# Kernel tuning notes

Measured on AMD Instinct MI355X. Metric: run time of the kernel, lower is better.

Reference implementation:

```python
import jax, jax.numpy as jnp
import numpy as np

T, D = 4096, 2048
H, DK, DV = 6, 256, 512        # heads, head_k_dim, head_v_dim (expand_v=2)
KD, VD = H * DK, H * DV        # 1536, 3072
KSZ = 4                        # conv_size
GEN = D // 8                   # generator reduction 8 -> 256
EPS = 1e-5                     # norm_eps


def setup_inputs() -> dict:
    key = jax.random.key(0)
    ks = jax.random.split(key, 12)
    std = 0.02
    p = lambda i, shape: jax.random.normal(ks[i], shape, jnp.float32) * std
    rng = np.random.default_rng(0)
    A = rng.uniform(0.0, 16.0, H).astype(np.float32)
    dt = np.exp(rng.uniform(0, 1, H) * (np.log(0.1) - np.log(0.001)) + np.log(0.001)).astype(np.float32)
    dt = np.clip(dt, 1e-4, None)
    inv_dt = (dt + np.log(-np.expm1(-dt))).astype(np.float32)
    return {
        'hidden_states': jax.random.normal(ks[0], (T, D), jnp.float32),
        'Wq': p(1, (D, KD)), 'Wk': p(2, (D, KD)), 'Wv': p(3, (D, VD)),
        'Wb': p(4, (D, H)), 'Wa': p(5, (D, H)), 'Wg': p(6, (D, VD)), 'Wo': p(7, (VD, D)),
        'A_log': jnp.asarray(np.log(A)), 'dt_bias': jnp.asarray(inv_dt),
        'conv_w': p(8, (VD, KSZ)), 'gen_w1': p(9, (D, GEN)), 'gen_w2': p(10, (GEN, KSZ)),
        'norm_w': jnp.ones((DV,), jnp.float32),
    }


def _l2norm(x):
    return x * jax.lax.rsqrt(jnp.sum(x * x, -1, keepdims=True) + 1e-6)


def reference(hidden_states, Wq, Wk, Wv, Wb, Wa, Wg, Wo, A_log, dt_bias, conv_w, gen_w1, gen_w2, norm_w):
    h = hidden_states[None]                             # [1,T,D]
    q = jax.nn.silu(h @ Wq)                             # [1,T,KD]
    k = jax.nn.silu(h @ Wk)
    x = h @ Wv                                          # [1,T,VD]
    # dynamic short convolution: per-token kernel added to static depthwise kernel
    dyn = jax.nn.silu(h @ gen_w1) @ gen_w2              # [1,T,KSZ]
    xpad = jnp.pad(x, ((0, 0), (KSZ - 1, 0), (0, 0)))   # causal padding
    v = jnp.zeros_like(x)
    for j in range(KSZ):
        v = v + (conv_w[None, None, :, j] + dyn[:, :, None, j]) * xpad[:, j:j + x.shape[1], :]
    v = jax.nn.silu(v)

    B = 1
    q = _l2norm(q.reshape(B, -1, H, DK))                # use_qk_l2norm_in_kernel=True
    k = _l2norm(k.reshape(B, -1, H, DK))
    v = v.reshape(B, -1, H, DV)
    beta = jax.nn.sigmoid(h @ Wb)                       # [1,T,H]
    g = -jnp.exp(A_log) * jax.nn.softplus(h @ Wa + dt_bias)  # [1,T,H] decay log-gates
    scale = DK ** -0.5

    def step(S, inp):                                   # gated delta rule recurrence
        qt, kt, vt, gt, bt = inp
        S = S * jnp.exp(gt)[..., None, None]            # [B,H,DK,DV]
        dv = (vt - jnp.einsum('bhk,bhkv->bhv', kt, S)) * bt[..., None]
        S = S + kt[..., :, None] * dv[..., None, :]
        ot = jnp.einsum('bhk,bhkv->bhv', qt, S) * scale
        return S, ot

    S0 = jnp.zeros((B, H, DK, DV), jnp.float32)
    tm = lambda a: jnp.moveaxis(a, 1, 0)                # time-major for scan
    _, o = jax.lax.scan(step, S0, (tm(q), tm(k), tm(v), tm(g), tm(beta)))
    o = jnp.moveaxis(o, 0, 1)                           # [1,T,H,DV]

    gate = (h @ Wg).reshape(B, -1, H, DV)
    rms = jax.lax.rsqrt(jnp.mean(o * o, -1, keepdims=True) + EPS)
    o = o * rms * norm_w * jax.nn.silu(gate)            # gated RMSNorm
    o = o.reshape(B, -1, VD) @ Wo                       # [1,T,D]
    return o[0]
```

## Files before the change

### kernel.cpp

```cpp
#include <hip/hip_runtime.h>
#include <hip/hip_bf16.h>
#include <math.h>

#define T_LEN 4096
#define DIM   2048
#define NH    6
#define DK    256
#define DVh   512
#define KD    1536
#define VD    3072
#define CK    64
#define NCHK  (T_LEN / CK)

typedef __attribute__((ext_vector_type(8))) short bf16x8;
typedef __attribute__((ext_vector_type(4))) float f32x4;

__device__ __forceinline__ float silu_f(float v){ return v / (1.f + __expf(-v)); }

__device__ __forceinline__ unsigned short f2bf(float f) {
  unsigned int u = __float_as_uint(f);
  unsigned int r = u + 0x7FFFu + ((u >> 16) & 1u);
  return (unsigned short)(r >> 16);
}
__device__ __forceinline__ float bf2f(unsigned short s) {
  return __uint_as_float(((unsigned int)s) << 16);
}

__device__ __forceinline__ void bar_lds() {
  __builtin_amdgcn_sched_barrier(0);
  asm volatile("s_waitcnt lgkmcnt(0)" ::: "memory");
  __builtin_amdgcn_s_barrier();
  __builtin_amdgcn_sched_barrier(0);
}

__global__ __launch_bounds__(256) void cast_bf16(
    const float* __restrict__ in, unsigned short* __restrict__ out)
{
  int i = blockIdx.x * 256 + threadIdx.x;
  float4 v4 = ((const float4*)in)[i];
  ushort4 o4;
  o4.x = f2bf(v4.x); o4.y = f2bf(v4.y); o4.z = f2bf(v4.z); o4.w = f2bf(v4.w);
  ((ushort4*)out)[i] = o4;
}

__global__ __launch_bounds__(256) void tcast(
    const float* __restrict__ in, unsigned short* __restrict__ out, int R, int Cn)
{
  __shared__ float tile[32][33];
  int bx = blockIdx.x * 32;
  int by = blockIdx.y * 32;
  int tx = threadIdx.x & 31, ty = threadIdx.x >> 5;
#pragma unroll
  for (int i = 0; i < 32; i += 8)
    tile[ty + i][tx] = in[(size_t)(by + ty + i) * Cn + bx + tx];
  __syncthreads();
#pragma unroll
  for (int i = 0; i < 32; i += 8)
    out[(size_t)(bx + ty + i) * R + by + tx] = f2bf(tile[tx][ty + i]);
}

__global__ __launch_bounds__(256) void gemm_bt_bf16(
    const unsigned short* __restrict__ A, const unsigned short* __restrict__ BT,
    void* __restrict__ Cout, int M, int N, int K, int act)
{
  __shared__ unsigned short As[128 * 32];
  __shared__ unsigned short Bs[128 * 32];
  const int tid = threadIdx.x;
  const int bm = blockIdx.y * 128, bn = blockIdx.x * 128;
  const int lane = tid & 63, wave = tid >> 6;
  const int wm = (wave >> 1) * 64, wn = (wave & 1) * 64;
  const int fr = lane & 15, kq = lane >> 4;

  f32x4 acc[4][4];
#pragma unroll
  for (int i = 0; i < 4; ++i)
#pragma unroll
    for (int j = 0; j < 4; ++j) acc[i][j] = (f32x4){0.f, 0.f, 0.f, 0.f};

  const int r0 = tid >> 2, c0 = (tid & 3) * 8;
  const int r1 = r0 + 64;

  for (int k0 = 0; k0 < K; k0 += 32) {
    __builtin_amdgcn_global_load_lds(
        (const __attribute__((address_space(1))) unsigned int*)(A + (size_t)(bm + r0) * K + k0 + c0),
        (__attribute__((address_space(3))) unsigned int*)(As + r0 * 32 + c0), 16, 0, 0);
    __builtin_amdgcn_global_load_lds(
        (const __attribute__((address_space(1))) unsigned int*)(A + (size_t)(bm + r1) * K + k0 + c0),
        (__attribute__((address_space(3))) unsigned int*)(As + r1 * 32 + c0), 16, 0, 0);
    __builtin_amdgcn_global_load_lds(
        (const __attribute__((address_space(1))) unsigned int*)(BT + (size_t)(bn + r0) * K + k0 + c0),
        (__attribute__((address_space(3))) unsigned int*)(Bs + r0 * 32 + c0), 16, 0, 0);
    __builtin_amdgcn_global_load_lds(
        (const __attribute__((address_space(1))) unsigned int*)(BT + (size_t)(bn + r1) * K + k0 + c0),
        (__attribute__((address_space(3))) unsigned int*)(Bs + r1 * 32 + c0), 16, 0, 0);
    __syncthreads();

    bf16x8 af[4], bfr[4];
#pragma unroll
    for (int i = 0; i < 4; ++i)
      af[i] = *(const bf16x8*)(As + (wm + i * 16 + fr) * 32 + kq * 8);
#pragma unroll
    for (int j = 0; j < 4; ++j)
      bfr[j] = *(const bf16x8*)(Bs + (wn + j * 16 + fr) * 32 + kq * 8);
#pragma unroll
    for (int i = 0; i < 4; ++i)
#pragma unroll
      for (int j = 0; j < 4; ++j)
        acc[i][j] = __builtin_amdgcn_mfma_f32_16x16x32_bf16(af[i], bfr[j], acc[i][j], 0, 0, 0);
    __syncthreads();
  }

  if (act == 2) {
    unsigned short* C = (unsigned short*)Cout;
#pragma unroll
    for (int i = 0; i < 4; ++i) {
      int rbase = bm + wm + i * 16 + kq * 4;
#pragma unroll
      for (int r = 0; r < 4; ++r) {
        size_t rowoff = (size_t)(rbase + r) * N + bn + wn + fr;
#pragma unroll
        for (int j = 0; j < 4; ++j) C[rowoff + j * 16] = f2bf(acc[i][j][r]);
      }
    }
  } else {
    float* C = (float*)Cout;
#pragma unroll
    for (int i = 0; i < 4; ++i) {
      int rbase = bm + wm + i * 16 + kq * 4;
#pragma unroll
      for (int r = 0; r < 4; ++r) {
        size_t rowoff = (size_t)(rbase + r) * N + bn + wn + fr;
#pragma unroll
        for (int j = 0; j < 4; ++j) {
          float v = acc[i][j][r];
          if (act == 1) v = silu_f(v);
          C[rowoff + j * 16] = v;
        }
      }
    }
  }
}

__global__ __launch_bounds__(256) void proj_dyn(
    const float* __restrict__ tg, const float* __restrict__ w2, float* __restrict__ dyn)
{
  int t = blockIdx.x, tid = threadIdx.x;
  float g = tg[(size_t)t * 256 + tid];
  float p[4];
#pragma unroll
  for (int j = 0; j < 4; ++j) p[j] = g * w2[tid * 4 + j];
#pragma unroll
  for (int j = 0; j < 4; ++j)
    for (int m = 32; m >= 1; m >>= 1) p[j] += __shfl_xor(p[j], m);
  __shared__ float red[4][4];
  if ((tid & 63) == 0) {
    int w = tid >> 6;
#pragma unroll
    for (int j = 0; j < 4; ++j) red[w][j] = p[j];
  }
  __syncthreads();
  if (tid < 4) dyn[(size_t)t * 4 + tid] = red[0][tid] + red[1][tid] + red[2][tid] + red[3][tid];
}

__global__ __launch_bounds__(256) void proj_bg(
    const float* __restrict__ h, const float* __restrict__ Wb, const float* __restrict__ Wa,
    const float* __restrict__ A_log, const float* __restrict__ dt_bias,
    float* __restrict__ beta, float* __restrict__ gout)
{
  int t = blockIdx.x, tid = threadIdx.x;
  float pb[6], pa[6];
#pragma unroll
  for (int j = 0; j < 6; ++j) { pb[j] = 0.f; pa[j] = 0.f; }
  for (int d = tid; d < DIM; d += 256) {
    float hv = h[(size_t)t * DIM + d];
#pragma unroll
    for (int j = 0; j < 6; ++j) {
      pb[j] += hv * Wb[d * 6 + j];
      pa[j] += hv * Wa[d * 6 + j];
    }
  }
#pragma unroll
  for (int j = 0; j < 6; ++j)
    for (int m = 32; m >= 1; m >>= 1) { pb[j] += __shfl_xor(pb[j], m); pa[j] += __shfl_xor(pa[j], m); }
  __shared__ float rb[4][6], ra[4][6];
  if ((tid & 63) == 0) {
    int w = tid >> 6;
#pragma unroll
    for (int j = 0; j < 6; ++j) { rb[w][j] = pb[j]; ra[w][j] = pa[j]; }
  }
  __syncthreads();
  if (tid < 6) {
    int j = tid;
    float sb = rb[0][j] + rb[1][j] + rb[2][j] + rb[3][j];
    float sa = ra[0][j] + ra[1][j] + ra[2][j] + ra[3][j];
    beta[(size_t)t * 6 + j] = 1.f / (1.f + expf(-sb));
    float z = sa + dt_bias[j];
    float sp = (z > 20.f) ? z : log1pf(expf(z));
    gout[(size_t)t * 6 + j] = -expf(A_log[j]) * sp;
  }
}

__global__ __launch_bounds__(256) void conv_kernel(
    const float* __restrict__ x, const float* __restrict__ dyn,
    const float* __restrict__ cw, float* __restrict__ v)
{
  int c = blockIdx.x * 256 + threadIdx.x;
  int t = blockIdx.y;
  float4 w4 = ((const float4*)cw)[c];
  float d0 = dyn[t * 4 + 0], d1 = dyn[t * 4 + 1], d2 = dyn[t * 4 + 2], d3 = dyn[t * 4 + 3];
  float acc = (w4.w + d3) * x[(size_t)t * VD + c];
  if (t >= 1) acc += (w4.z + d2) * x[(size_t)(t - 1) * VD + c];
  if (t >= 2) acc += (w4.y + d1) * x[(size_t)(t - 2) * VD + c];
  if (t >= 3) acc += (w4.x + d0) * x[(size_t)(t - 3) * VD + c];
  v[(size_t)t * VD + c] = silu_f(acc);
}

__global__ __launch_bounds__(64) void l2norm_qk(
    float* __restrict__ q, float* __restrict__ k)
{
  size_t base = (size_t)blockIdx.x * 256;
  int tid = threadIdx.x;
  float4 qv = ((float4*)(q + base))[tid];
  float4 kv = ((float4*)(k + base))[tid];
  float sq = qv.x*qv.x + qv.y*qv.y + qv.z*qv.z + qv.w*qv.w;
  float sk = kv.x*kv.x + kv.y*kv.y + kv.z*kv.z + kv.w*kv.w;
  for (int m = 32; m >= 1; m >>= 1) { sq += __shfl_xor(sq, m); sk += __shfl_xor(sk, m); }
  float rq = rsqrtf(sq + 1e-6f) * 0.0625f;
  float rk = rsqrtf(sk + 1e-6f);
  qv.x *= rq; qv.y *= rq; qv.z *= rq; qv.w *= rq;
  kv.x *= rk; kv.y *= rk; kv.z *= rk; kv.w *= rk;
  ((float4*)(q + base))[tid] = qv;
  ((float4*)(k + base))[tid] = kv;
}

__global__ __launch_bounds__(64) void cumsum_g(
    const float* __restrict__ g, float* __restrict__ c, float* __restrict__ gammas)
{
  int ch = blockIdx.x, h = blockIdx.y;
  int t0 = ch * CK;
  int lane = threadIdx.x;
  float cum = g[(size_t)(t0 + lane) * 6 + h];
  for (int off = 1; off < 64; off <<= 1) {
    float n = __shfl_up(cum, off);
    if (lane >= off) cum += n;
  }
  c[(size_t)h * T_LEN + t0 + lane] = cum;
  if (lane == 63) gammas[h * NCHK + ch] = __expf(cum);
}

__global__ __launch_bounds__(384) void scale_kq(
    const float* __restrict__ q, const float* __restrict__ k, const float* __restrict__ c,
    unsigned short* __restrict__ Qb, unsigned short* __restrict__ Kb)
{
  int t = blockIdx.x;
  int tid = threadIdx.x;
  int h = tid >> 6;
  float w1 = __expf(c[(size_t)h * T_LEN + t]);
  size_t off = (size_t)t * KD + tid * 4;
  float4 qv = *(const float4*)(q + off);
  float4 kv = *(const float4*)(k + off);
  ushort4 qo, ko;
  qo.x = f2bf(w1 * qv.x); qo.y = f2bf(w1 * qv.y); qo.z = f2bf(w1 * qv.z); qo.w = f2bf(w1 * qv.w);
  ko.x = f2bf(w1 * kv.x); ko.y = f2bf(w1 * kv.y); ko.z = f2bf(w1 * kv.z); ko.w = f2bf(w1 * kv.w);
  *(ushort4*)(Qb + off) = qo;
  *(ushort4*)(Kb + off) = ko;
}

__global__ __launch_bounds__(256) void make_khT(
    const float* __restrict__ k, const float* __restrict__ c,
    unsigned short* __restrict__ KhT)
{
  int ch = blockIdx.x, h = blockIdx.y;
  int t0 = ch * CK;
  int tt = threadIdx.x & 63, ks = threadIdx.x >> 6;
  float cend = c[(size_t)h * T_LEN + t0 + 63];
  float w2 = __expf(cend - c[(size_t)h * T_LEN + t0 + tt]);
  size_t obase = ((size_t)(h * NCHK + ch)) * DK * CK;
#pragma unroll 8
  for (int kb2 = 0; kb2 < 64; ++kb2) {
    int kk = ks * 64 + kb2;
    float kv = k[(size_t)(t0 + tt) * KD + h * 256 + kk];
    KhT[obase + (size_t)kk * CK + tt] = f2bf(w2 * kv);
  }
}

__global__ __launch_bounds__(256) void chunk_lp(
    const float* __restrict__ q, const float* __restrict__ k,
    const float* __restrict__ c, const float* __restrict__ beta,
    float* __restrict__ Lg, unsigned short* __restrict__ Pm)
{
  const int ch = blockIdx.x, h = blockIdx.y;
  const int t0 = ch * CK;
  const int tid = threadIdx.x;
  const int w = tid >> 6, lane = tid & 63, fr = lane & 15, kq = lane >> 4;
  __shared__ unsigned short kb[64][264];
  __shared__ unsigned short qb[64][264];
  __shared__ float cs[64], bs[64];
#pragma unroll
  for (int i = 0; i < 16; ++i) {
    int fi = tid + i * 256;
    int r = fi >> 6, d4 = fi & 63;
    float4 kv = *(const float4*)(k + (size_t)(t0 + r) * KD + h * 256 + d4 * 4);
    float4 qv = *(const float4*)(q + (size_t)(t0 + r) * KD + h * 256 + d4 * 4);
    ushort4 k4, q4;
    k4.x = f2bf(kv.x); k4.y = f2bf(kv.y); k4.z = f2bf(kv.z); k4.w = f2bf(kv.w);
    q4.x = f2bf(qv.x); q4.y = f2bf(qv.y); q4.z = f2bf(qv.z); q4.w = f2bf(qv.w);
    *(ushort4*)&kb[r][d4 * 4] = k4;
    *(ushort4*)&qb[r][d4 * 4] = q4;
  }
  if (tid < 64) {
    cs[tid] = c[(size_t)h * T_LEN + t0 + tid];
    bs[tid] = beta[(size_t)(t0 + tid) * 6 + h];
  }
  __syncthreads();

  f32x4 akk[4], aqk[4];
#pragma unroll
  for (int j = 0; j < 4; ++j) { akk[j] = (f32x4){0,0,0,0}; aqk[j] = (f32x4){0,0,0,0}; }
#pragma unroll
  for (int kt = 0; kt < 8; ++kt) {
    bf16x8 ak = *(const bf16x8*)&kb[16 * w + fr][kt * 32 + kq * 8];
    bf16x8 aq = *(const bf16x8*)&qb[16 * w + fr][kt * 32 + kq * 8];
#pragma unroll
    for (int j = 0; j < 4; ++j) {
      bf16x8 b = *(const bf16x8*)&kb[j * 16 + fr][kt * 32 + kq * 8];
      akk[j] = __builtin_amdgcn_mfma_f32_16x16x32_bf16(ak, b, akk[j], 0, 0, 0);
      aqk[j] = __builtin_amdgcn_mfma_f32_16x16x32_bf16(aq, b, aqk[j], 0, 0, 0);
    }
  }
  size_t base = ((size_t)(h * NCHK + ch)) * CK * CK;
#pragma unroll
  for (int j = 0; j < 4; ++j) {
#pragma unroll
    for (int r = 0; r < 4; ++r) {
      int t = 16 * w + kq * 4 + r, col = j * 16 + fr;
      float e = __expf(fminf(cs[t] - cs[col], 0.f));
      Lg[base + t * 64 + col] = (col < t) ? bs[t] * e * akk[j][r] : 0.f;
      Pm[base + t * 64 + col] = f2bf((col <= t) ? e * aqk[j][r] : 0.f);
    }
  }
}

__global__ __launch_bounds__(64) void tri_inv(
    const float* __restrict__ Lg, const float* __restrict__ beta,
    unsigned short* __restrict__ Tm)
{
  const int ch = blockIdx.x, h = blockIdx.y;
  const size_t base = ((size_t)(h * NCHK + ch)) * CK * CK;
  const int j = threadIdx.x;
  __shared__ float Ll[64][65];
  __shared__ float Tl[64][65];
  for (int t = 0; t < 64; ++t) Ll[t][j] = Lg[base + t * 64 + j];
  __syncthreads();
  for (int t = 0; t < 64; ++t) {
    float s;
    if (j > t) s = 0.f;
    else if (j == t) s = 1.f;
    else {
      s = 0.f;
      for (int m = j; m < t; ++m) s -= Ll[t][m] * Tl[m][j];
    }
    Tl[t][j] = s;
  }
  float bj = beta[(size_t)(ch * 64 + j) * 6 + h];
  for (int t = 0; t < 64; ++t) Tm[base + t * 64 + j] = f2bf(Tl[t][j] * bj);
}

__global__ __launch_bounds__(256) void scan_chunk(
    const unsigned short* __restrict__ Kb,
    const unsigned short* __restrict__ Qb,
    const unsigned short* __restrict__ KhT,
    const unsigned short* __restrict__ Tm,
    const unsigned short* __restrict__ Pm,
    const float* __restrict__ gammas,
    float* __restrict__ VO)
{
  const int h = blockIdx.y, sl = blockIdx.x;
  const int tid = threadIdx.x;
  const int w = tid >> 6, lane = tid & 63;
  const int fr = lane & 15, kq = lane >> 4;

  __shared__ unsigned short S0h[16][264];
  __shared__ unsigned short S0l[16][264];
  __shared__ unsigned short XT[16][72];
  __shared__ unsigned short DVT[16][72];

  f32x4 st[4];
#pragma unroll
  for (int i = 0; i < 4; ++i) st[i] = (f32x4){0.f, 0.f, 0.f, 0.f};

  const int colg = h * DVh + sl * 16 + fr;
  const size_t hc0 = (size_t)h * NCHK;

  {
    int zr = tid >> 4;
    int zc = (tid & 15) * 16;
    ushort4 z; z.x = 0; z.y = 0; z.z = 0; z.w = 0;
#pragma unroll
    for (int u = 0; u < 4; ++u) {
      *(ushort4*)&S0h[zr][zc + 4 * u] = z;
      *(ushort4*)&S0l[zr][zc + 4 * u] = z;
    }
  }

  bf16x8 kfA[8], kfB[8], qfA[8], qfB[8];
  float vlA[4], vlB[4];

#define PREF_KQV(KF, QF, VL, chn) do { \
    const unsigned short* krow_ = Kb + (size_t)((chn) * CK + 16 * w + fr) * KD + h * 256 + kq * 8; \
    const unsigned short* qrow_ = Qb + (size_t)((chn) * CK + 16 * w + fr) * KD + h * 256 + kq * 8; \
    _Pragma("unroll") \
    for (int kt = 0; kt < 8; ++kt) { \
      KF[kt] = *(const bf16x8*)(krow_ + kt * 32); \
      QF[kt] = *(const bf16x8*)(qrow_ + kt * 32); } \
    _Pragma("unroll") \
    for (int r = 0; r < 4; ++r) VL[r] = VO[(size_t)((chn) * CK + 16 * w + kq * 4 + r) * VD + colg]; \
  } while (0)

#define CHUNK_BODY(chx, KF, QF, VL, KFN, QFN, VLN) do { \
    const int ch_ = (chx); \
    const int t0_ = ch_ * CK; \
    const size_t cb_ = hc0 + ch_; \
    bf16x8 tf[2], pf[2]; \
    { const unsigned short* trow_ = Tm + (cb_ * CK + 16 * w + fr) * CK + kq * 8; \
      const unsigned short* prow_ = Pm + (cb_ * CK + 16 * w + fr) * CK + kq * 8; \
      tf[0] = *(const bf16x8*)(trow_); tf[1] = *(const bf16x8*)(trow_ + 32); \
      pf[0] = *(const bf16x8*)(prow_); pf[1] = *(const bf16x8*)(prow_ + 32); } \
    bf16x8 hfr[4][2]; \
    _Pragma("unroll") \
    for (int i = 0; i < 4; ++i) { \
      const unsigned short* hrow_ = KhT + (cb_ * DK + 64 * w + 16 * i + fr) * CK + kq * 8; \
      hfr[i][0] = *(const bf16x8*)(hrow_); hfr[i][1] = *(const bf16x8*)(hrow_ + 32); } \
    const float gam_ = gammas[cb_]; \
     \
    { const int chn_ = (ch_ + 1 < NCHK) ? ch_ + 1 : ch_; PREF_KQV(KFN, QFN, VLN, chn_); } \
     \
     \
    f32x4 oh = (f32x4){0.f,0.f,0.f,0.f}, ol = (f32x4){0.f,0.f,0.f,0.f}; \
    { f32x4 yh = (f32x4){0.f,0.f,0.f,0.f}, yl = (f32x4){0.f,0.f,0.f,0.f}; \
      _Pragma("unroll") \
      for (int kt = 0; kt < 8; ++kt) { \
        bf16x8 bh_ = *(const bf16x8*)&S0h[fr][kt * 32 + kq * 8]; \
        bf16x8 bl_ = *(const bf16x8*)&S0l[fr][kt * 32 + kq * 8]; \
        yh = __builtin_amdgcn_mfma_f32_16x16x32_bf16(KF[kt], bh_, yh, 0, 0, 0); \
        yl = __builtin_amdgcn_mfma_f32_16x16x32_bf16(KF[kt], bl_, yl, 0, 0, 0); \
        oh = __builtin_amdgcn_mfma_f32_16x16x32_bf16(QF[kt], bh_, oh, 0, 0, 0); \
        ol = __builtin_amdgcn_mfma_f32_16x16x32_bf16(QF[kt], bl_, ol, 0, 0, 0); } \
      ushort4 x4; \
      x4.x = f2bf(VL[0] - (yh[0] + yl[0])); \
      x4.y = f2bf(VL[1] - (yh[1] + yl[1])); \
      x4.z = f2bf(VL[2] - (yh[2] + yl[2])); \
      x4.w = f2bf(VL[3] - (yh[3] + yl[3])); \
      *(ushort4*)&XT[fr][16 * w + kq * 4] = x4; } \
    bar_lds(); \
     \
    { f32x4 d = (f32x4){0.f,0.f,0.f,0.f}; \
      bf16x8 b0_ = *(const bf16x8*)&XT[fr][kq * 8]; \
      bf16x8 b1_ = *(const bf16x8*)&XT[fr][32 + kq * 8]; \
      d = __builtin_amdgcn_mfma_f32_16x16x32_bf16(tf[0], b0_, d, 0, 0, 0); \
      d = __builtin_amdgcn_mfma_f32_16x16x32_bf16(tf[1], b1_, d, 0, 0, 0); \
      ushort4 d4; \
      d4.x = f2bf(d[0]); d4.y = f2bf(d[1]); d4.z = f2bf(d[2]); d4.w = f2bf(d[3]); \
      *(ushort4*)&DVT[fr][16 * w + kq * 4] = d4; } \
    bar_lds(); \
     \
     \
    { bf16x8 dv0_ = *(const bf16x8*)&DVT[fr][kq * 8]; \
      bf16x8 dv1_ = *(const bf16x8*)&DVT[fr][32 + kq * 8]; \
      f32x4 op = (f32x4){0.f,0.f,0.f,0.f}; \
      op = __builtin_amdgcn_mfma_f32_16x16x32_bf16(pf[0], dv0_, op, 0, 0, 0); \
      op = __builtin_amdgcn_mfma_f32_16x16x32_bf16(pf[1], dv1_, op, 0, 0, 0); \
      _Pragma("unroll") \
      for (int r = 0; r < 4; ++r) \
        VO[(size_t)(t0_ + 16 * w + kq * 4 + r) * VD + colg] = oh[r] + ol[r] + op[r]; \
      _Pragma("unroll") \
      for (int i = 0; i < 4; ++i) { \
        st[i][0] *= gam_; st[i][1] *= gam_; st[i][2] *= gam_; st[i][3] *= gam_; \
        st[i] = __builtin_amdgcn_mfma_f32_16x16x32_bf16(hfr[i][0], dv0_, st[i], 0, 0, 0); \
        st[i] = __builtin_amdgcn_mfma_f32_16x16x32_bf16(hfr[i][1], dv1_, st[i], 0, 0, 0); \
        ushort4 hi4, lo4; \
        { float s0 = st[i][0], s1 = st[i][1], s2 = st[i][2], s3 = st[i][3]; \
          hi4.x = f2bf(s0); lo4.x = f2bf(s0 - bf2f(hi4.x)); \
          hi4.y = f2bf(s1); lo4.y = f2bf(s1 - bf2f(hi4.y)); \
          hi4.z = f2bf(s2); lo4.z = f2bf(s2 - bf2f(hi4.z)); \
          hi4.w = f2bf(s3); lo4.w = f2bf(s3 - bf2f(hi4.w)); } \
        *(ushort4*)&S0h[fr][64 * w + 16 * i + kq * 4] = hi4; \
        *(ushort4*)&S0l[fr][64 * w + 16 * i + kq * 4] = lo4; } } \
    bar_lds(); \
  } while (0)

  PREF_KQV(kfA, qfA, vlA, 0);
  __syncthreads();
  for (int ch = 0; ch < NCHK; ch += 2) {
    CHUNK_BODY(ch,     kfA, qfA, vlA, kfB, qfB, vlB);
    CHUNK_BODY(ch + 1, kfB, qfB, vlB, kfA, qfA, vlA);
  }
#undef CHUNK_BODY
#undef PREF_KQV
}

__global__ __launch_bounds__(256) void norm_gate(
    const float* __restrict__ o, const unsigned short* __restrict__ gate,
    const float* __restrict__ nw, unsigned short* __restrict__ out)
{
  int th = blockIdx.x, tid = threadIdx.x;
  size_t base = (size_t)th * DVh;
  float x0 = o[base + tid], x1 = o[base + 256 + tid];
  float ss = x0 * x0 + x1 * x1;
  for (int m = 32; m >= 1; m >>= 1) ss += __shfl_xor(ss, m);
  __shared__ float red[4];
  if ((tid & 63) == 0) red[tid >> 6] = ss;
  __syncthreads();
  float rms = rsqrtf((red[0] + red[1] + red[2] + red[3]) * (1.f / 512.f) + 1e-5f);
  float g0 = bf2f(gate[base + tid]), g1 = bf2f(gate[base + 256 + tid]);
  out[base + tid]       = f2bf(x0 * rms * nw[tid]       * silu_f(g0));
  out[base + 256 + tid] = f2bf(x1 * rms * nw[tid + 256] * silu_f(g1));
}

extern "C" void kernel_launch(void* const* d_in, const int* in_sizes, int n_in,
                              void* d_out, int out_size, void* d_ws, size_t ws_size,
                              hipStream_t stream)
{
  const float* h       = (const float*)d_in[0];
  const float* Wq      = (const float*)d_in[1];
  const float* Wk      = (const float*)d_in[2];
  const float* Wv      = (const float*)d_in[3];
  const float* Wb      = (const float*)d_in[4];
  const float* Wa      = (const float*)d_in[5];
  const float* Wg      = (const float*)d_in[6];
  const float* Wo      = (const float*)d_in[7];
  const float* A_log   = (const float*)d_in[8];
  const float* dt_bias = (const float*)d_in[9];
  const float* conv_w  = (const float*)d_in[10];
  const float* gen_w1  = (const float*)d_in[11];
  const float* gen_w2  = (const float*)d_in[12];
  const float* norm_w  = (const float*)d_in[13];
  float* out = (float*)d_out;

  const size_t TK = (size_t)T_LEN * KD, TV = (size_t)T_LEN * VD, TD = (size_t)T_LEN * DIM;

  float* ws   = (float*)d_ws;
  float* q    = ws;
  float* k    = q    + TK;
  float* x    = k    + TK;
  float* v    = x    + TV;
  float* tg   = v    + TV;
  float* dyn  = tg   + (size_t)T_LEN * 256;
  float* beta = dyn  + (size_t)T_LEN * 4;
  float* g    = beta + (size_t)T_LEN * 6;
  float* c    = g    + (size_t)T_LEN * 6;
  float* gam  = c    + (size_t)NH * T_LEN;
  float* fend = gam  + 512;
  unsigned short* bh      = (unsigned short*)fend;
  unsigned short* wT      = bh      + TD;
  unsigned short* gate_bf = wT      + (size_t)DIM * VD;
  unsigned short* go_bf   = gate_bf + TV;
  unsigned short* Kb_s  = bh;
  unsigned short* Qb_s  = (unsigned short*)x;
  unsigned short* KhT_s = Qb_s + TK;
  unsigned short* Tm_s  = KhT_s + TK;
  unsigned short* Pm_s  = Tm_s + (size_t)NH * NCHK * CK * CK;
  float* Lg = (float*)go_bf;

  dim3 blk(256);
  cast_bf16<<<(TD / 4) / 256, blk, 0, stream>>>(h, bh);
  tcast<<<dim3(KD / 32, DIM / 32), blk, 0, stream>>>(Wq, wT, DIM, KD);
  gemm_bt_bf16<<<dim3(KD / 128, T_LEN / 128), blk, 0, stream>>>(bh, wT, q, T_LEN, KD, DIM, 1);
  tcast<<<dim3(KD / 32, DIM / 32), blk, 0, stream>>>(Wk, wT, DIM, KD);
  gemm_bt_bf16<<<dim3(KD / 128, T_LEN / 128), blk, 0, stream>>>(bh, wT, k, T_LEN, KD, DIM, 1);
  tcast<<<dim3(VD / 32, DIM / 32), blk, 0, stream>>>(Wv, wT, DIM, VD);
  gemm_bt_bf16<<<dim3(VD / 128, T_LEN / 128), blk, 0, stream>>>(bh, wT, x, T_LEN, VD, DIM, 0);
  tcast<<<dim3(VD / 32, DIM / 32), blk, 0, stream>>>(Wg, wT, DIM, VD);
  gemm_bt_bf16<<<dim3(VD / 128, T_LEN / 128), blk, 0, stream>>>(bh, wT, gate_bf, T_LEN, VD, DIM, 2);
  tcast<<<dim3(256 / 32, DIM / 32), blk, 0, stream>>>(gen_w1, wT, DIM, 256);
  gemm_bt_bf16<<<dim3(256 / 128, T_LEN / 128), blk, 0, stream>>>(bh, wT, tg, T_LEN, 256, DIM, 1);

  proj_dyn<<<T_LEN, blk, 0, stream>>>(tg, gen_w2, dyn);
  proj_bg<<<T_LEN, blk, 0, stream>>>(h, Wb, Wa, A_log, dt_bias, beta, g);
  conv_kernel<<<dim3(VD / 256, T_LEN), blk, 0, stream>>>(x, dyn, conv_w, v);
  l2norm_qk<<<T_LEN * NH, 64, 0, stream>>>(q, k);

  cumsum_g<<<dim3(NCHK, NH), 64, 0, stream>>>(g, c, gam);
  scale_kq<<<T_LEN, 384, 0, stream>>>(q, k, c, Qb_s, Kb_s);
  make_khT<<<dim3(NCHK, NH), blk, 0, stream>>>(k, c, KhT_s);
  chunk_lp<<<dim3(NCHK, NH), blk, 0, stream>>>(q, k, c, beta, Lg, Pm_s);
  tri_inv<<<dim3(NCHK, NH), 64, 0, stream>>>(Lg, beta, Tm_s);

  scan_chunk<<<dim3(DVh / 16, NH), blk, 0, stream>>>(Kb_s, Qb_s, KhT_s, Tm_s, Pm_s, gam, v);

  norm_gate<<<T_LEN * NH, blk, 0, stream>>>(v, gate_bf, norm_w, go_bf);
  tcast<<<dim3(DIM / 32, VD / 32), blk, 0, stream>>>(Wo, wT, VD, DIM);
  gemm_bt_bf16<<<dim3(DIM / 128, T_LEN / 128), blk, 0, stream>>>(go_bf, wT, out, T_LEN, DIM, VD, 0);
}
```

Before: 1.050 ms.

## Split scan_chunk K-reduction across two wave groups with 512-thread blocks

The chunked delta-rule scan kernel now launches 512 threads per block. Two groups of four waves each handle half of the 256-wide key dimension, and their partial K·S and Q·S products are combined through shared-memory buffers. The T-matrix and P-matrix multiplies are divided between the two groups, each wave updates half as many state tiles, and s_setprio is raised around the MFMA-heavy sections. The goal is to shorten the serial per-chunk critical path of this low-occupancy kernel (192 blocks), at the cost of an extra barrier plus LDS reduction traffic per chunk.

```diff
diff --git a/kernel.cpp b/kernel.cpp
--- a/kernel.cpp
+++ b/kernel.cpp
@@ -366,7 +366,7 @@
   for (int t = 0; t < 64; ++t) Tm[base + t * 64 + j] = f2bf(Tl[t][j] * bj);
 }
 
-__global__ __launch_bounds__(256) void scan_chunk(
+__global__ __launch_bounds__(512, 2) void scan_chunk(
     const unsigned short* __restrict__ Kb,
     const unsigned short* __restrict__ Qb,
     const unsigned short* __restrict__ KhT,
@@ -378,103 +378,117 @@
   const int h = blockIdx.y, sl = blockIdx.x;
   const int tid = threadIdx.x;
   const int w = tid >> 6, lane = tid & 63;
+  const int tw = w & 3, kg = w >> 2;
   const int fr = lane & 15, kq = lane >> 4;
 
   __shared__ unsigned short S0h[16][264];
   __shared__ unsigned short S0l[16][264];
   __shared__ unsigned short XT[16][72];
   __shared__ unsigned short DVT[16][72];
-
-  f32x4 st[4];
-#pragma unroll
-  for (int i = 0; i < 4; ++i) st[i] = (f32x4){0.f, 0.f, 0.f, 0.f};
+  __shared__ float PY[2][4][16][20];
+  __shared__ float PO[2][4][16][20];
+
+  f32x4 st[2];
+  st[0] = (f32x4){0.f, 0.f, 0.f, 0.f};
+  st[1] = (f32x4){0.f, 0.f, 0.f, 0.f};
 
   const int colg = h * DVh + sl * 16 + fr;
   const size_t hc0 = (size_t)h * NCHK;
 
   {
-    int zr = tid >> 4;
-    int zc = (tid & 15) * 16;
+    int zr = tid >> 5;
+    int zc = (tid & 31) * 8;
     ushort4 z; z.x = 0; z.y = 0; z.z = 0; z.w = 0;
-#pragma unroll
-    for (int u = 0; u < 4; ++u) {
-      *(ushort4*)&S0h[zr][zc + 4 * u] = z;
-      *(ushort4*)&S0l[zr][zc + 4 * u] = z;
-    }
-  }
-
-  bf16x8 kfA[8], kfB[8], qfA[8], qfB[8];
+    *(ushort4*)&S0h[zr][zc]     = z;
+    *(ushort4*)&S0h[zr][zc + 4] = z;
+    *(ushort4*)&S0l[zr][zc]     = z;
+    *(ushort4*)&S0l[zr][zc + 4] = z;
+  }
+
+  bf16x8 kfA[4], kfB[4], qfA[4], qfB[4];
   float vlA[4], vlB[4];
 
-#define PREF_KQV(KF, QF, VL, chn) do { \
-    const unsigned short* krow_ = Kb + (size_t)((chn) * CK + 16 * w + fr) * KD + h * 256 + kq * 8; \
-    const unsigned short* qrow_ = Qb + (size_t)((chn) * CK + 16 * w + fr) * KD + h * 256 + kq * 8; \
+#define PREF(KF, QF, VL, chn) do { \
+    const unsigned short* kr_ = Kb + (size_t)((chn) * CK + 16 * tw + fr) * KD + h * 256 + kg * 128 + kq * 8; \
+    const unsigned short* qr_ = Qb + (size_t)((chn) * CK + 16 * tw + fr) * KD + h * 256 + kg * 128 + kq * 8; \
     _Pragma("unroll") \
-    for (int kt = 0; kt < 8; ++kt) { \
-      KF[kt] = *(const bf16x8*)(krow_ + kt * 32); \
-      QF[kt] = *(const bf16x8*)(qrow_ + kt * 32); } \
-    _Pragma("unroll") \
-    for (int r = 0; r < 4; ++r) VL[r] = VO[(size_t)((chn) * CK + 16 * w + kq * 4 + r) * VD + colg]; \
+    for (int kt = 0; kt < 4; ++kt) { \
+      KF[kt] = *(const bf16x8*)(kr_ + kt * 32); \
+      QF[kt] = *(const bf16x8*)(qr_ + kt * 32); } \
+    if (kg == 0) { \
+      _Pragma("unroll") \
+      for (int r = 0; r < 4; ++r) VL[r] = VO[(size_t)((chn) * CK + 16 * tw + kq * 4 + r) * VD + colg]; } \
   } while (0)
 
-#define CHUNK_BODY(chx, KF, QF, VL, KFN, QFN, VLN) do { \
+#define BODY(chx, KF, QF, VL, KFN, QFN, VLN) do { \
     const int ch_ = (chx); \
     const int t0_ = ch_ * CK; \
     const size_t cb_ = hc0 + ch_; \
-    bf16x8 tf[2], pf[2]; \
-    { const unsigned short* trow_ = Tm + (cb_ * CK + 16 * w + fr) * CK + kq * 8; \
-      const unsigned short* prow_ = Pm + (cb_ * CK + 16 * w + fr) * CK + kq * 8; \
-      tf[0] = *(const bf16x8*)(trow_); tf[1] = *(const bf16x8*)(trow_ + 32); \
-      pf[0] = *(const bf16x8*)(prow_); pf[1] = *(const bf16x8*)(prow_ + 32); } \
-    bf16x8 hfr[4][2]; \
+     \
+    bf16x8 tpf[2]; \
+    { const unsigned short* b_ = (kg == 0 ? Tm : Pm) + (cb_ * CK + 16 * tw + fr) * CK + kq * 8; \
+      tpf[0] = *(const bf16x8*)(b_); tpf[1] = *(const bf16x8*)(b_ + 32); } \
+    bf16x8 hfr[2][2]; \
     _Pragma("unroll") \
-    for (int i = 0; i < 4; ++i) { \
-      const unsigned short* hrow_ = KhT + (cb_ * DK + 64 * w + 16 * i + fr) * CK + kq * 8; \
-      hfr[i][0] = *(const bf16x8*)(hrow_); hfr[i][1] = *(const bf16x8*)(hrow_ + 32); } \
+    for (int i = 0; i < 2; ++i) { \
+      const unsigned short* hr_ = KhT + (cb_ * DK + 32 * w + 16 * i + fr) * CK + kq * 8; \
+      hfr[i][0] = *(const bf16x8*)(hr_); hfr[i][1] = *(const bf16x8*)(hr_ + 32); } \
     const float gam_ = gammas[cb_]; \
+    { const int chn_ = (ch_ + 1 < NCHK) ? ch_ + 1 : ch_; PREF(KFN, QFN, VLN, chn_); } \
      \
-    { const int chn_ = (ch_ + 1 < NCHK) ? ch_ + 1 : ch_; PREF_KQV(KFN, QFN, VLN, chn_); } \
-     \
-     \
-    f32x4 oh = (f32x4){0.f,0.f,0.f,0.f}, ol = (f32x4){0.f,0.f,0.f,0.f}; \
-    { f32x4 yh = (f32x4){0.f,0.f,0.f,0.f}, yl = (f32x4){0.f,0.f,0.f,0.f}; \
+    f32x4 yt, ot; \
+    { f32x4 yh = (f32x4){0.f,0.f,0.f,0.f}, yl = yh, oh = yh, ol = yh; \
+      __builtin_amdgcn_s_setprio(1); \
       _Pragma("unroll") \
-      for (int kt = 0; kt < 8; ++kt) { \
-        bf16x8 bh_ = *(const bf16x8*)&S0h[fr][kt * 32 + kq * 8]; \
-        bf16x8 bl_ = *(const bf16x8*)&S0l[fr][kt * 32 + kq * 8]; \
+      for (int kt = 0; kt < 4; ++kt) { \
+        const int ka_ = (kg * 4 + kt) * 32 + kq * 8; \
+        bf16x8 bh_ = *(const bf16x8*)&S0h[fr][ka_]; \
+        bf16x8 bl_ = *(const bf16x8*)&S0l[fr][ka_]; \
         yh = __builtin_amdgcn_mfma_f32_16x16x32_bf16(KF[kt], bh_, yh, 0, 0, 0); \
         yl = __builtin_amdgcn_mfma_f32_16x16x32_bf16(KF[kt], bl_, yl, 0, 0, 0); \
         oh = __builtin_amdgcn_mfma_f32_16x16x32_bf16(QF[kt], bh_, oh, 0, 0, 0); \
         ol = __builtin_amdgcn_mfma_f32_16x16x32_bf16(QF[kt], bl_, ol, 0, 0, 0); } \
+      __builtin_amdgcn_s_setprio(0); \
+      yt = yh + yl; ot = oh + ol; } \
+    *(f32x4*)&PY[kg][tw][fr][kq * 4] = yt; \
+    *(f32x4*)&PO[kg][tw][fr][kq * 4] = ot; \
+    bar_lds();    \
+    if (kg == 0) { \
+      f32x4 yo = *(const f32x4*)&PY[1][tw][fr][kq * 4]; \
       ushort4 x4; \
-      x4.x = f2bf(VL[0] - (yh[0] + yl[0])); \
-      x4.y = f2bf(VL[1] - (yh[1] + yl[1])); \
-      x4.z = f2bf(VL[2] - (yh[2] + yl[2])); \
-      x4.w = f2bf(VL[3] - (yh[3] + yl[3])); \
-      *(ushort4*)&XT[fr][16 * w + kq * 4] = x4; } \
-    bar_lds(); \
+      x4.x = f2bf(VL[0] - (yt[0] + yo[0])); \
+      x4.y = f2bf(VL[1] - (yt[1] + yo[1])); \
+      x4.z = f2bf(VL[2] - (yt[2] + yo[2])); \
+      x4.w = f2bf(VL[3] - (yt[3] + yo[3])); \
+      *(ushort4*)&XT[fr][16 * tw + kq * 4] = x4; \
+    } else { \
+      f32x4 oo = *(const f32x4*)&PO[0][tw][fr][kq * 4]; \
+      ot[0] += oo[0]; ot[1] += oo[1]; ot[2] += oo[2]; ot[3] += oo[3]; } \
+    bar_lds();    \
      \
-    { f32x4 d = (f32x4){0.f,0.f,0.f,0.f}; \
+    if (kg == 0) { \
+      f32x4 d = (f32x4){0.f,0.f,0.f,0.f}; \
       bf16x8 b0_ = *(const bf16x8*)&XT[fr][kq * 8]; \
       bf16x8 b1_ = *(const bf16x8*)&XT[fr][32 + kq * 8]; \
-      d = __builtin_amdgcn_mfma_f32_16x16x32_bf16(tf[0], b0_, d, 0, 0, 0); \
-      d = __builtin_amdgcn_mfma_f32_16x16x32_bf16(tf[1], b1_, d, 0, 0, 0); \
+      d = __builtin_amdgcn_mfma_f32_16x16x32_bf16(tpf[0], b0_, d, 0, 0, 0); \
+      d = __builtin_amdgcn_mfma_f32_16x16x32_bf16(tpf[1], b1_, d, 0, 0, 0); \
       ushort4 d4; \
       d4.x = f2bf(d[0]); d4.y = f2bf(d[1]); d4.z = f2bf(d[2]); d4.w = f2bf(d[3]); \
-      *(ushort4*)&DVT[fr][16 * w + kq * 4] = d4; } \
-    bar_lds(); \
-     \
+      *(ushort4*)&DVT[fr][16 * tw + kq * 4] = d4; } \
+    bar_lds();    \
      \
     { bf16x8 dv0_ = *(const bf16x8*)&DVT[fr][kq * 8]; \
       bf16x8 dv1_ = *(const bf16x8*)&DVT[fr][32 + kq * 8]; \
-      f32x4 op = (f32x4){0.f,0.f,0.f,0.f}; \
-      op = __builtin_amdgcn_mfma_f32_16x16x32_bf16(pf[0], dv0_, op, 0, 0, 0); \
-      op = __builtin_amdgcn_mfma_f32_16x16x32_bf16(pf[1], dv1_, op, 0, 0, 0); \
+      if (kg == 1) { \
+        f32x4 op = (f32x4){0.f,0.f,0.f,0.f}; \
+        op = __builtin_amdgcn_mfma_f32_16x16x32_bf16(tpf[0], dv0_, op, 0, 0, 0); \
+        op = __builtin_amdgcn_mfma_f32_16x16x32_bf16(tpf[1], dv1_, op, 0, 0, 0); \
+        _Pragma("unroll") \
+        for (int r = 0; r < 4; ++r) \
+          VO[(size_t)(t0_ + 16 * tw + kq * 4 + r) * VD + colg] = ot[r] + op[r]; } \
+      __builtin_amdgcn_s_setprio(1); \
       _Pragma("unroll") \
-      for (int r = 0; r < 4; ++r) \
-        VO[(size_t)(t0_ + 16 * w + kq * 4 + r) * VD + colg] = oh[r] + ol[r] + op[r]; \
-      _Pragma("unroll") \
-      for (int i = 0; i < 4; ++i) { \
+      for (int i = 0; i < 2; ++i) { \
         st[i][0] *= gam_; st[i][1] *= gam_; st[i][2] *= gam_; st[i][3] *= gam_; \
         st[i] = __builtin_amdgcn_mfma_f32_16x16x32_bf16(hfr[i][0], dv0_, st[i], 0, 0, 0); \
         st[i] = __builtin_amdgcn_mfma_f32_16x16x32_bf16(hfr[i][1], dv1_, st[i], 0, 0, 0); \
@@ -484,19 +498,20 @@
           hi4.y = f2bf(s1); lo4.y = f2bf(s1 - bf2f(hi4.y)); \
           hi4.z = f2bf(s2); lo4.z = f2bf(s2 - bf2f(hi4.z)); \
           hi4.w = f2bf(s3); lo4.w = f2bf(s3 - bf2f(hi4.w)); } \
-        *(ushort4*)&S0h[fr][64 * w + 16 * i + kq * 4] = hi4; \
-        *(ushort4*)&S0l[fr][64 * w + 16 * i + kq * 4] = lo4; } } \
-    bar_lds(); \
+        *(ushort4*)&S0h[fr][32 * w + 16 * i + kq * 4] = hi4; \
+        *(ushort4*)&S0l[fr][32 * w + 16 * i + kq * 4] = lo4; } \
+      __builtin_amdgcn_s_setprio(0); } \
+    bar_lds();    \
   } while (0)
 
-  PREF_KQV(kfA, qfA, vlA, 0);
+  PREF(kfA, qfA, vlA, 0);
   __syncthreads();
   for (int ch = 0; ch < NCHK; ch += 2) {
-    CHUNK_BODY(ch,     kfA, qfA, vlA, kfB, qfB, vlB);
-    CHUNK_BODY(ch + 1, kfB, qfB, vlB, kfA, qfA, vlA);
-  }
-#undef CHUNK_BODY
-#undef PREF_KQV
+    BODY(ch,     kfA, qfA, vlA, kfB, qfB, vlB);
+    BODY(ch + 1, kfB, qfB, vlB, kfA, qfA, vlA);
+  }
+#undef BODY
+#undef PREF
 }
 
 __global__ __launch_bounds__(256) void norm_gate(
@@ -586,7 +601,7 @@
   chunk_lp<<<dim3(NCHK, NH), blk, 0, stream>>>(q, k, c, beta, Lg, Pm_s);
   tri_inv<<<dim3(NCHK, NH), 64, 0, stream>>>(Lg, beta, Tm_s);
 
-  scan_chunk<<<dim3(DVh / 16, NH), blk, 0, stream>>>(Kb_s, Qb_s, KhT_s, Tm_s, Pm_s, gam, v);
+  scan_chunk<<<dim3(DVh / 16, NH), 512, 0, stream>>>(Kb_s, Qb_s, KhT_s, Tm_s, Pm_s, gam, v);
 
   norm_gate<<<T_LEN * NH, blk, 0, stream>>>(v, gate_bf, norm_w, go_bf);
   tcast<<<dim3(DIM / 32, VD / 32), blk, 0, stream>>>(Wo, wT, VD, DIM);
```

Measured after the change: 1.035 ms. Within noise of the previous version (-1.5%).
